# Kernel optimization log

Hardware: AMD Instinct MI355X
Metric: run time of the kernel (lower is better)

## Reference

```python
import jax, jax.numpy as jnp
import numpy as np

B, T, D = 4, 1024, 1024       # batch, tokens, emb_size
E, K, F_EXP = 8, 2, 1024      # num_expert, num_expert_active, expert_size
NUM_BLOCK = 12


def setup_inputs() -> dict:
    key = jax.random.key(0)
    k_x, k_b, k_r, k_1, k_2 = jax.random.split(key, 5)
    x = jax.random.normal(k_x, (B, T, D), dtype=jnp.float32)
    auxfree_bias = jax.random.normal(k_b, (E,), dtype=jnp.float32) * 0.1
    router_w = jax.random.normal(k_r, (E, D), dtype=jnp.float32) * 0.02
    # GroupedLinear weight{i}: [out_features, in_features], applied as x @ W^T
    w1 = jax.random.normal(k_1, (E, F_EXP, D), dtype=jnp.float32) * 0.02
    w2 = jax.random.normal(k_2, (E, D, F_EXP), dtype=jnp.float32) * (0.02 / np.sqrt(2.0 * NUM_BLOCK))
    return {"x": x, "auxfree_bias": auxfree_bias, "router_w": router_w, "w1": w1, "w2": w2}


def reference(x, auxfree_bias, router_w, w1, w2):
    # --- routing: top-k on bias-adjusted DETACHED logits, gather raw logits ---
    logits = jnp.einsum("btd,ed->bte", x, router_w)              # [B,T,E]
    biased = jax.lax.stop_gradient(logits) + auxfree_bias        # bias only affects selection
    _, idx = jax.lax.top_k(biased, K)                            # [B,T,K] int32
    gathered = jnp.take_along_axis(logits, idx, axis=-1)         # [B,T,K]
    probs = jax.nn.softmax(gathered, axis=-1)                    # [B,T,K]

    # combine weights per expert: sum_k probs_k * 1[idx_k == e]  -> [B,T,E]
    combine = jnp.sum(jax.nn.one_hot(idx, E, dtype=x.dtype) * probs[..., None], axis=2)

    # --- experts: out = sum_e combine_e * (gelu(x W1_e^T) W2_e^T) ---
    # (dense per-expert reference for the dispatch -> grouped GEMM -> combine pipeline;
    #  tokens with combine weight 0 contribute nothing, matching the sparse original)
    out = jnp.zeros_like(x)
    for e in range(E):
        h = jax.nn.gelu(jnp.einsum("btd,fd->btf", x, w1[e]), approximate=False)
        out = out + combine[:, :, e:e + 1] * jnp.einsum("btf,df->btd", h, w2[e])
    return out
```

## Files before the change

### kernel.cpp

```cpp
#include <hip/hip_runtime.h>
#include <hip/hip_bf16.h>

#define D_DIM 1024
#define F_DIM 1024
#define NTOK  4096
#define NEXP  8
#define CAP   4096
#define NGRP_X (NTOK * D_DIM / 8)
#define NGRP_W (NEXP * F_DIM * D_DIM / 8)

typedef __attribute__((ext_vector_type(8))) short bf16x8;
typedef __attribute__((ext_vector_type(4))) float f32x4;
typedef __attribute__((ext_vector_type(8))) unsigned short u16x8;

__device__ __forceinline__ unsigned short f2bf(float f) {
    unsigned int u = __float_as_uint(f);
    u = u + 0x7fffu + ((u >> 16) & 1u);
    return (unsigned short)(u >> 16);
}

__device__ __forceinline__ void async_copy16(void* lds, const void* gsrc) {
    __builtin_amdgcn_global_load_lds(
        (const __attribute__((address_space(1))) unsigned int*)gsrc,
        (__attribute__((address_space(3))) unsigned int*)lds, 16, 0, 0);
}

__global__ __launch_bounds__(256) void cvt3_kernel(
    const float* __restrict__ x, const float* __restrict__ w1, const float* __restrict__ w2,
    unsigned short* __restrict__ xb, unsigned short* __restrict__ w1b,
    unsigned short* __restrict__ w2b)
{
    long g = (long)blockIdx.x * 256 + threadIdx.x;
    const float* src; unsigned short* dst; long o;
    if (g < NGRP_X)            { src = x;  dst = xb;  o = g; }
    else if (g < NGRP_X + NGRP_W) { src = w1; dst = w1b; o = g - NGRP_X; }
    else                       { src = w2; dst = w2b; o = g - NGRP_X - NGRP_W; }
    size_t i = (size_t)o * 8;
    const float4* p = (const float4*)(src + i);
    float4 a = p[0], b = p[1];
    u16x8 r;
    r[0] = f2bf(a.x); r[1] = f2bf(a.y); r[2] = f2bf(a.z); r[3] = f2bf(a.w);
    r[4] = f2bf(b.x); r[5] = f2bf(b.y); r[6] = f2bf(b.z); r[7] = f2bf(b.w);
    *(u16x8*)(dst + i) = r;
}

__global__ __launch_bounds__(256) void logits_kernel(
    const float* __restrict__ x, const float* __restrict__ rw,
    float* __restrict__ logits)
{
    const int wave = threadIdx.x >> 6, lane = threadIdx.x & 63;
    const int t = blockIdx.x * 4 + wave;
    double s[NEXP];
    #pragma unroll
    for (int e = 0; e < NEXP; ++e) s[e] = 0.0;
    const float* xp = x + (size_t)t * D_DIM;
    for (int kk = 0; kk < D_DIM; kk += 64) {
        float xv = xp[kk + lane];
        #pragma unroll
        for (int e = 0; e < NEXP; ++e)
            s[e] += (double)xv * (double)rw[e * D_DIM + kk + lane];
    }
    #pragma unroll
    for (int e = 0; e < NEXP; ++e) {
        double v = s[e];
        for (int off = 32; off; off >>= 1) v += __shfl_xor(v, off, 64);
        s[e] = v;
    }
    if (lane == 0) {
        #pragma unroll
        for (int e = 0; e < NEXP; ++e) logits[(size_t)t * NEXP + e] = (float)s[e];
    }
}

__global__ __launch_bounds__(256) void assign_kernel(
    const float* __restrict__ logits, const float* __restrict__ bias,
    int* counts, int* list, int* pairEP, float* pairW)
{
    __shared__ int lcnt[NEXP];
    __shared__ int lbase[NEXP];
    const int tid = threadIdx.x;
    const int t = blockIdx.x * 256 + tid;
    if (tid < NEXP) lcnt[tid] = 0;
    __syncthreads();

    float lg[NEXP], b2[NEXP];
    #pragma unroll
    for (int e = 0; e < NEXP; ++e) {
        lg[e] = logits[(size_t)t * NEXP + e];
        b2[e] = lg[e] + bias[e];
    }
    int i0 = 0; float b0v = b2[0], l0v = lg[0];
    #pragma unroll
    for (int e = 1; e < NEXP; ++e)
        if (b2[e] > b0v) { b0v = b2[e]; l0v = lg[e]; i0 = e; }
    int i1 = -1; float b1v = 0.f, l1v = 0.f;
    #pragma unroll
    for (int e = 0; e < NEXP; ++e) {
        if (e == i0) continue;
        bool take = (i1 < 0) || (b2[e] > b1v);
        if (take) { i1 = e; b1v = b2[e]; l1v = lg[e]; }
    }
    float m = fmaxf(l0v, l1v);
    float e0 = expf(l0v - m), e1 = expf(l1v - m);
    float inv = 1.0f / (e0 + e1);

    int lp0 = atomicAdd(&lcnt[i0], 1);
    int lp1 = atomicAdd(&lcnt[i1], 1);
    __syncthreads();
    if (tid < NEXP) lbase[tid] = atomicAdd(&counts[tid], lcnt[tid]);
    __syncthreads();

    int p0 = lbase[i0] + lp0;
    int p1 = lbase[i1] + lp1;
    list[i0 * CAP + p0] = t;
    list[i1 * CAP + p1] = t;
    pairEP[2 * t]     = (p0 << 3) | i0;
    pairEP[2 * t + 1] = (p1 << 3) | i1;
    pairW[2 * t]      = e0 * inv;
    pairW[2 * t + 1]  = e1 * inv;
}

#define STAGE(AB, BB, k0)                                                   \
    do {                                                                    \
        _Pragma("unroll")                                                   \
        for (int i = 0; i < 4; ++i)                                         \
            async_copy16(&AB[(wave * 4 + i) * 512], ap[i] + (k0));          \
        _Pragma("unroll")                                                   \
        for (int i = 0; i < 2; ++i)                                         \
            async_copy16(&BB[(wave * 2 + i) * 512], bp_[i] + (k0));         \
    } while (0)

#define COMPUTE(AB, BB)                                                     \
    do {                                                                    \
        _Pragma("unroll")                                                   \
        for (int kk = 0; kk < 2; ++kk) {                                    \
            bf16x8 af[4], bfv[2];                                           \
            const int phys = (((kk * 4) + (lane >> 4)) ^ (lane & 7)) * 8;   \
            _Pragma("unroll")                                               \
            for (int m = 0; m < 4; ++m)                                     \
                af[m] = *(const bf16x8*)&AB[(wr * 64 + m * 16 + (lane & 15)) * 64 + phys]; \
            _Pragma("unroll")                                               \
            for (int n = 0; n < 2; ++n)                                     \
                bfv[n] = *(const bf16x8*)&BB[(wc * 32 + n * 16 + (lane & 15)) * 64 + phys]; \
            _Pragma("unroll")                                               \
            for (int m = 0; m < 4; ++m)                                     \
                _Pragma("unroll")                                           \
                for (int n = 0; n < 2; ++n)                                 \
                    acc[m][n] = __builtin_amdgcn_mfma_f32_16x16x32_bf16(af[m], bfv[n], acc[m][n], 0, 0, 0); \
        }                                                                   \
    } while (0)

__global__ __launch_bounds__(256) void gemm1_kernel(
    const unsigned short* __restrict__ xb,
    const unsigned short* __restrict__ w1b,
    const int* __restrict__ counts,
    const int* __restrict__ list,
    unsigned short* __restrict__ H)
{
    const int bid = blockIdx.x;
    const int e  = bid & 7;
    const int s  = bid >> 3;
    const int rb = s >> 4;
    const int ne = counts[e];
    if (rb * 128 >= ne) return;
    const int row0 = rb * 128;
    const int n0 = (s & 15) * 64;
    int hbase = 0;
    #pragma unroll
    for (int ee = 0; ee < NEXP; ++ee) if (ee < e) hbase += counts[ee];

    __shared__ __align__(16) unsigned short As[128 * 64];
    __shared__ __align__(16) unsigned short Bs[64 * 64];
    __shared__ int toks[128];

    const int tid = threadIdx.x;
    if (tid < 128) {
        int i = row0 + tid;
        if (i >= ne) i = ne - 1;
        toks[tid] = list[e * CAP + i];
    }
    __syncthreads();

    const int wave = tid >> 6, lane = tid & 63;
    const int wr = wave >> 1, wc = wave & 1;

    const int lr  = lane >> 3;
    const int swz = ((lane & 7) ^ lr) * 8;
    const unsigned short* ap[4];
    const unsigned short* bp_[2];
    const unsigned short* wbase = w1b + (size_t)e * F_DIM * D_DIM;
    #pragma unroll
    for (int i = 0; i < 4; ++i)
        ap[i] = xb + (size_t)toks[wave * 32 + i * 8 + lr] * D_DIM + swz;
    #pragma unroll
    for (int i = 0; i < 2; ++i)
        bp_[i] = wbase + (size_t)(n0 + wave * 16 + i * 8 + lr) * D_DIM + swz;

    f32x4 acc[4][2];
    #pragma unroll
    for (int m = 0; m < 4; ++m)
        #pragma unroll
        for (int n = 0; n < 2; ++n) acc[m][n] = (f32x4){0.f, 0.f, 0.f, 0.f};

    for (int k0 = 0; k0 < D_DIM; k0 += 64) {
        STAGE(As, Bs, k0);
        __syncthreads();
        COMPUTE(As, Bs);
        __syncthreads();
    }

    #pragma unroll
    for (int m = 0; m < 4; ++m) {
        #pragma unroll
        for (int j = 0; j < 4; ++j) {
            int ri = wr * 64 + m * 16 + (lane >> 4) * 4 + j;
            int i = row0 + ri;
            if (i < ne) {
                unsigned short* hp = H + (size_t)(hbase + i) * F_DIM + n0 + wc * 32;
                #pragma unroll
                for (int n = 0; n < 2; ++n) {
                    float v = acc[m][n][j];
                    float g = 0.5f * v * (1.0f + erff(v * 0.70710678118654752f));
                    hp[n * 16 + (lane & 15)] = f2bf(g);
                }
            }
        }
    }
}

__global__ __launch_bounds__(256) void gemm2_kernel(
    const unsigned short* __restrict__ H,
    const unsigned short* __restrict__ w2b,
    const int* __restrict__ counts,
    float* __restrict__ O2)
{
    const int bid = blockIdx.x;
    const int e  = bid & 7;
    const int s  = bid >> 3;
    const int rb = s >> 4;
    const int ne = counts[e];
    if (rb * 128 >= ne) return;
    const int row0 = rb * 128;
    const int n0 = (s & 15) * 64;
    int hbase = 0;
    #pragma unroll
    for (int ee = 0; ee < NEXP; ++ee) if (ee < e) hbase += counts[ee];

    __shared__ __align__(16) unsigned short As[128 * 64];
    __shared__ __align__(16) unsigned short Bs[64 * 64];

    const int tid = threadIdx.x;
    const int wave = tid >> 6, lane = tid & 63;
    const int wr = wave >> 1, wc = wave & 1;

    const int lr  = lane >> 3;
    const int swz = ((lane & 7) ^ lr) * 8;
    const unsigned short* ap[4];
    const unsigned short* bp_[2];
    const unsigned short* wbase = w2b + (size_t)e * D_DIM * F_DIM;
    #pragma unroll
    for (int i = 0; i < 4; ++i)
        ap[i] = H + (size_t)(hbase + row0 + wave * 32 + i * 8 + lr) * F_DIM + swz;
    #pragma unroll
    for (int i = 0; i < 2; ++i)
        bp_[i] = wbase + (size_t)(n0 + wave * 16 + i * 8 + lr) * F_DIM + swz;

    f32x4 acc[4][2];
    #pragma unroll
    for (int m = 0; m < 4; ++m)
        #pragma unroll
        for (int n = 0; n < 2; ++n) acc[m][n] = (f32x4){0.f, 0.f, 0.f, 0.f};

    for (int k0 = 0; k0 < F_DIM; k0 += 64) {
        STAGE(As, Bs, k0);
        __syncthreads();
        COMPUTE(As, Bs);
        __syncthreads();
    }

    #pragma unroll
    for (int m = 0; m < 4; ++m) {
        #pragma unroll
        for (int j = 0; j < 4; ++j) {
            int ri = wr * 64 + m * 16 + (lane >> 4) * 4 + j;
            int i = row0 + ri;
            if (i < ne) {
                float* op = O2 + (size_t)(hbase + i) * D_DIM + n0 + wc * 32;
                #pragma unroll
                for (int n = 0; n < 2; ++n)
                    op[n * 16 + (lane & 15)] = acc[m][n][j];
            }
        }
    }
}

__global__ __launch_bounds__(256) void combine_kernel(
    const float* __restrict__ O2, const int* __restrict__ counts,
    const int* __restrict__ pairEP, const float* __restrict__ pairW,
    float* __restrict__ out)
{
    const int t = blockIdx.x;
    const int tid = threadIdx.x;
    int offs[NEXP];
    int a = 0;
    #pragma unroll
    for (int e = 0; e < NEXP; ++e) { offs[e] = a; a += counts[e]; }
    int ep0 = pairEP[2 * t], ep1 = pairEP[2 * t + 1];
    float w0 = pairW[2 * t], w1 = pairW[2 * t + 1];
    int e0 = ep0 & 7, e1 = ep1 & 7, o0 = 0, o1 = 0;
    #pragma unroll
    for (int e = 0; e < NEXP; ++e) {
        if (e == e0) o0 = offs[e];
        if (e == e1) o1 = offs[e];
    }
    size_t r0 = (size_t)(o0 + (ep0 >> 3)) * D_DIM;
    size_t r1 = (size_t)(o1 + (ep1 >> 3)) * D_DIM;
    float4 va = *(const float4*)(O2 + r0 + tid * 4);
    float4 vb = *(const float4*)(O2 + r1 + tid * 4);
    float4 r;
    r.x = w0 * va.x + w1 * vb.x;
    r.y = w0 * va.y + w1 * vb.y;
    r.z = w0 * va.z + w1 * vb.z;
    r.w = w0 * va.w + w1 * vb.w;
    *(float4*)(out + (size_t)t * D_DIM + tid * 4) = r;
}

extern "C" void kernel_launch(void* const* d_in, const int* in_sizes, int n_in,
                              void* d_out, int out_size, void* d_ws, size_t ws_size,
                              hipStream_t stream)
{
    const float* x    = (const float*)d_in[0];
    const float* bias = (const float*)d_in[1];
    const float* rw   = (const float*)d_in[2];
    const float* w1   = (const float*)d_in[3];
    const float* w2   = (const float*)d_in[4];
    float* out = (float*)d_out;

    char* ws = (char*)d_ws;
    unsigned short* w2b = (unsigned short*)(ws);
    unsigned short* Hb  = (unsigned short*)(ws + 16777216);
    float*          O2  = (float*)        (ws + 33816576);
    unsigned short* xb  = (unsigned short*)(ws + 33816576);
    unsigned short* w1b = (unsigned short*)(ws + 33816576 + 8388608);
    char* tail = ws + 33816576 + 34078720;
    float* logits = (float*)(tail);
    int*   list   = (int*)(tail + 131072);
    int*   pairEP = (int*)(tail + 262144);
    float* pairW  = (float*)(tail + 294912);
    int*   counts = (int*)(tail + 327680);

    hipMemsetAsync(counts, 0, 64, stream);

    cvt3_kernel<<<(NGRP_X + 2 * NGRP_W) / 256, 256, 0, stream>>>(x, w1, w2, xb, w1b, w2b);
    logits_kernel<<<NTOK / 4, 256, 0, stream>>>(x, rw, logits);
    assign_kernel<<<NTOK / 256, 256, 0, stream>>>(logits, bias, counts, list, pairEP, pairW);
    gemm1_kernel<<<4096, 256, 0, stream>>>(xb, w1b, counts, list, Hb);
    gemm2_kernel<<<4096, 256, 0, stream>>>(Hb, w2b, counts, O2);
    combine_kernel<<<NTOK, 256, 0, stream>>>(O2, counts, pairEP, pairW, out);
}
```

Baseline: 218.2 us.

## Fuse bf16 conversion into routing and GEMM B-tile loads, drop cvt kernel

Removes the standalone fp32-to-bf16 conversion kernel. The x conversion moves into the logits kernel, and the weight conversion happens inside each GEMM block while it stages the B tile: fp32 is loaded, rounded, and written to LDS synchronously instead of through async global-to-LDS copies. This saves a full pass over the 64MB of fp32 weights plus the bf16 writeback. The cost is that every row block re-reads twice as many fp32 weight bytes, and the async B copy is replaced by register-staged loads.

```diff
diff --git a/kernel.cpp b/kernel.cpp
--- a/kernel.cpp
+++ b/kernel.cpp
@@ -6,8 +6,6 @@
 #define NTOK  4096
 #define NEXP  8
 #define CAP   4096
-#define NGRP_X (NTOK * D_DIM / 8)
-#define NGRP_W (NEXP * F_DIM * D_DIM / 8)
 
 typedef __attribute__((ext_vector_type(8))) short bf16x8;
 typedef __attribute__((ext_vector_type(4))) float f32x4;
@@ -25,28 +23,9 @@
         (__attribute__((address_space(3))) unsigned int*)lds, 16, 0, 0);
 }
 
-__global__ __launch_bounds__(256) void cvt3_kernel(
-    const float* __restrict__ x, const float* __restrict__ w1, const float* __restrict__ w2,
-    unsigned short* __restrict__ xb, unsigned short* __restrict__ w1b,
-    unsigned short* __restrict__ w2b)
-{
-    long g = (long)blockIdx.x * 256 + threadIdx.x;
-    const float* src; unsigned short* dst; long o;
-    if (g < NGRP_X)            { src = x;  dst = xb;  o = g; }
-    else if (g < NGRP_X + NGRP_W) { src = w1; dst = w1b; o = g - NGRP_X; }
-    else                       { src = w2; dst = w2b; o = g - NGRP_X - NGRP_W; }
-    size_t i = (size_t)o * 8;
-    const float4* p = (const float4*)(src + i);
-    float4 a = p[0], b = p[1];
-    u16x8 r;
-    r[0] = f2bf(a.x); r[1] = f2bf(a.y); r[2] = f2bf(a.z); r[3] = f2bf(a.w);
-    r[4] = f2bf(b.x); r[5] = f2bf(b.y); r[6] = f2bf(b.z); r[7] = f2bf(b.w);
-    *(u16x8*)(dst + i) = r;
-}
-
 __global__ __launch_bounds__(256) void logits_kernel(
     const float* __restrict__ x, const float* __restrict__ rw,
-    float* __restrict__ logits)
+    float* __restrict__ logits, unsigned short* __restrict__ xb)
 {
     const int wave = threadIdx.x >> 6, lane = threadIdx.x & 63;
     const int t = blockIdx.x * 4 + wave;
@@ -54,8 +33,10 @@
     #pragma unroll
     for (int e = 0; e < NEXP; ++e) s[e] = 0.0;
     const float* xp = x + (size_t)t * D_DIM;
+    unsigned short* xo = xb + (size_t)t * D_DIM;
     for (int kk = 0; kk < D_DIM; kk += 64) {
         float xv = xp[kk + lane];
+        xo[kk + lane] = f2bf(xv);
         #pragma unroll
         for (int e = 0; e < NEXP; ++e)
             s[e] += (double)xv * (double)rw[e * D_DIM + kk + lane];
@@ -120,14 +101,27 @@
     pairW[2 * t + 1]  = e1 * inv;
 }
 
-#define STAGE(AB, BB, k0)                                                   \
+#define STAGE_A(AB, k0)                                                     \
     do {                                                                    \
         _Pragma("unroll")                                                   \
         for (int i = 0; i < 4; ++i)                                         \
             async_copy16(&AB[(wave * 4 + i) * 512], ap[i] + (k0));          \
+    } while (0)
+
+#define STAGE_B_F32(BB, k0)                                                 \
+    do {                                                                    \
         _Pragma("unroll")                                                   \
-        for (int i = 0; i < 2; ++i)                                         \
-            async_copy16(&BB[(wave * 2 + i) * 512], bp_[i] + (k0));         \
+        for (int i = 0; i < 2; ++i) {                                       \
+            const float* src = bpf[i] + (k0);                               \
+            float4 v0 = *(const float4*)(src);                              \
+            float4 v1 = *(const float4*)(src + 4);                          \
+            u16x8 rbv;                                                      \
+            rbv[0] = f2bf(v0.x); rbv[1] = f2bf(v0.y);                       \
+            rbv[2] = f2bf(v0.z); rbv[3] = f2bf(v0.w);                       \
+            rbv[4] = f2bf(v1.x); rbv[5] = f2bf(v1.y);                       \
+            rbv[6] = f2bf(v1.z); rbv[7] = f2bf(v1.w);                       \
+            *(u16x8*)&BB[(wave * 2 + i) * 512 + lane * 8] = rbv;            \
+        }                                                                   \
     } while (0)
 
 #define COMPUTE(AB, BB)                                                     \
@@ -152,7 +146,7 @@
 
 __global__ __launch_bounds__(256) void gemm1_kernel(
     const unsigned short* __restrict__ xb,
-    const unsigned short* __restrict__ w1b,
+    const float* __restrict__ w1,
     const int* __restrict__ counts,
     const int* __restrict__ list,
     unsigned short* __restrict__ H)
@@ -185,16 +179,16 @@
     const int wr = wave >> 1, wc = wave & 1;
 
     const int lr  = lane >> 3;
-    const int swz = ((lane & 7) ^ lr) * 8;
+    const int s8  = (lane & 7) ^ lr;
     const unsigned short* ap[4];
-    const unsigned short* bp_[2];
-    const unsigned short* wbase = w1b + (size_t)e * F_DIM * D_DIM;
+    const float* bpf[2];
+    const float* wbase = w1 + (size_t)e * F_DIM * D_DIM;
     #pragma unroll
     for (int i = 0; i < 4; ++i)
-        ap[i] = xb + (size_t)toks[wave * 32 + i * 8 + lr] * D_DIM + swz;
+        ap[i] = xb + (size_t)toks[wave * 32 + i * 8 + lr] * D_DIM + s8 * 8;
     #pragma unroll
     for (int i = 0; i < 2; ++i)
-        bp_[i] = wbase + (size_t)(n0 + wave * 16 + i * 8 + lr) * D_DIM + swz;
+        bpf[i] = wbase + (size_t)(n0 + wave * 16 + i * 8 + lr) * D_DIM + s8 * 8;
 
     f32x4 acc[4][2];
     #pragma unroll
@@ -203,7 +197,8 @@
         for (int n = 0; n < 2; ++n) acc[m][n] = (f32x4){0.f, 0.f, 0.f, 0.f};
 
     for (int k0 = 0; k0 < D_DIM; k0 += 64) {
-        STAGE(As, Bs, k0);
+        STAGE_A(As, k0);
+        STAGE_B_F32(Bs, k0);
         __syncthreads();
         COMPUTE(As, Bs);
         __syncthreads();
@@ -230,7 +225,7 @@
 
 __global__ __launch_bounds__(256) void gemm2_kernel(
     const unsigned short* __restrict__ H,
-    const unsigned short* __restrict__ w2b,
+    const float* __restrict__ w2,
     const int* __restrict__ counts,
     float* __restrict__ O2)
 {
@@ -254,16 +249,16 @@
     const int wr = wave >> 1, wc = wave & 1;
 
     const int lr  = lane >> 3;
-    const int swz = ((lane & 7) ^ lr) * 8;
+    const int s8  = (lane & 7) ^ lr;
     const unsigned short* ap[4];
-    const unsigned short* bp_[2];
-    const unsigned short* wbase = w2b + (size_t)e * D_DIM * F_DIM;
+    const float* bpf[2];
+    const float* wbase = w2 + (size_t)e * D_DIM * F_DIM;
     #pragma unroll
     for (int i = 0; i < 4; ++i)
-        ap[i] = H + (size_t)(hbase + row0 + wave * 32 + i * 8 + lr) * F_DIM + swz;
+        ap[i] = H + (size_t)(hbase + row0 + wave * 32 + i * 8 + lr) * F_DIM + s8 * 8;
     #pragma unroll
     for (int i = 0; i < 2; ++i)
-        bp_[i] = wbase + (size_t)(n0 + wave * 16 + i * 8 + lr) * F_DIM + swz;
+        bpf[i] = wbase + (size_t)(n0 + wave * 16 + i * 8 + lr) * F_DIM + s8 * 8;
 
     f32x4 acc[4][2];
     #pragma unroll
@@ -272,7 +267,8 @@
         for (int n = 0; n < 2; ++n) acc[m][n] = (f32x4){0.f, 0.f, 0.f, 0.f};
 
     for (int k0 = 0; k0 < F_DIM; k0 += 64) {
-        STAGE(As, Bs, k0);
+        STAGE_A(As, k0);
+        STAGE_B_F32(Bs, k0);
         __syncthreads();
         COMPUTE(As, Bs);
         __syncthreads();
@@ -337,12 +333,10 @@
     float* out = (float*)d_out;
 
     char* ws = (char*)d_ws;
-    unsigned short* w2b = (unsigned short*)(ws);
-    unsigned short* Hb  = (unsigned short*)(ws + 16777216);
-    float*          O2  = (float*)        (ws + 33816576);
-    unsigned short* xb  = (unsigned short*)(ws + 33816576);
-    unsigned short* w1b = (unsigned short*)(ws + 33816576 + 8388608);
-    char* tail = ws + 33816576 + 34078720;
+    unsigned short* xb = (unsigned short*)(ws);
+    unsigned short* Hb = (unsigned short*)(ws + 8388608);
+    float*          O2 = (float*)        (ws + 8388608 + 17039360);
+    char* tail = ws + 8388608 + 17039360 + 34078720;
     float* logits = (float*)(tail);
     int*   list   = (int*)(tail + 131072);
     int*   pairEP = (int*)(tail + 262144);
@@ -351,10 +345,9 @@
 
     hipMemsetAsync(counts, 0, 64, stream);
 
-    cvt3_kernel<<<(NGRP_X + 2 * NGRP_W) / 256, 256, 0, stream>>>(x, w1, w2, xb, w1b, w2b);
-    logits_kernel<<<NTOK / 4, 256, 0, stream>>>(x, rw, logits);
+    logits_kernel<<<NTOK / 4, 256, 0, stream>>>(x, rw, logits, xb);
     assign_kernel<<<NTOK / 256, 256, 0, stream>>>(logits, bias, counts, list, pairEP, pairW);
-    gemm1_kernel<<<4096, 256, 0, stream>>>(xb, w1b, counts, list, Hb);
-    gemm2_kernel<<<4096, 256, 0, stream>>>(Hb, w2b, counts, O2);
+    gemm1_kernel<<<4096, 256, 0, stream>>>(xb, w1, counts, list, Hb);
+    gemm2_kernel<<<4096, 256, 0, stream>>>(Hb, w2, counts, O2);
     combine_kernel<<<NTOK, 256, 0, stream>>>(O2, counts, pairEP, pairW, out);
 }
```

After: 222.9 us. +2.1%, slower.
